# Performance work log

Measured on AMD Instinct MI355X. Metric: run time of the kernel, lower is better.

Reference implementation:

```python
import jax, jax.numpy as jnp
import numpy as np

IN_SIZE = 1024
OUT_SIZE = 4096
LOGN = 12          # ceil(log2(max(in,out)))
N = 1 << LOGN      # 4096
BATCH = 8192


def setup_inputs() -> dict:
    key = jax.random.key(0)
    k1, k2, k3 = jax.random.split(key, 3)
    # kaiming_uniform on [2*logN, N]: fan_in = N, bound = sqrt(6/fan_in)
    bound = float(np.sqrt(6.0 / N))
    learned_params = jax.random.uniform(k1, (2 * LOGN, N), minval=-bound, maxval=bound, dtype=jnp.float32)
    inp = jax.random.normal(k2, (BATCH, IN_SIZE), dtype=jnp.float32)
    # np.random.permutation(N)[:out_size]
    out_row_indices = jax.random.permutation(k3, N)[:OUT_SIZE].astype(jnp.int32)
    return {"input": inp, "learned_params": learned_params, "out_row_indices": out_row_indices}


def reference(input, learned_params, out_row_indices):
    # Build B = prod_i (diag(p[2i]) + P_i @ diag(p[2i+1])), P_i[j, j^2^i] = 1.
    # (P_i @ diag(d) @ B)[j, :] = d[j^2^i] * B[j^2^i, :], so each layer is a
    # row-scale + xor-permuted row-scale of B (same math as the dense matmul chain).
    B = jnp.eye(N, dtype=input.dtype)
    for i in range(LOGN):
        perm = jnp.arange(N) ^ (1 << i)  # static per layer
        B = learned_params[2 * i][:, None] * B + learned_params[2 * i + 1][perm][:, None] * B[perm]
    layer_matrix = B[out_row_indices, :IN_SIZE]   # [out_size, in_size]
    return input @ layer_matrix.T                  # [batch, out_size]
```

## Files before the change

kernel.cpp:

```cpp
#include <hip/hip_runtime.h>


typedef float f4 __attribute__((ext_vector_type(4)));
typedef float f2 __attribute__((ext_vector_type(2)));
typedef int   i4 __attribute__((ext_vector_type(4)));

__device__ __forceinline__ int swz(int e) {
    return e ^ (((e >> 5) & 3) << 2);
}

template<int CTRL>
__device__ __forceinline__ float dppx(float x) {
    int xi = __builtin_bit_cast(int, x);
    int r  = __builtin_amdgcn_update_dpp(xi, xi, CTRL, 0xF, 0xF, true);
    return __builtin_bit_cast(float, r);
}

__global__ void __launch_bounds__(256) bfly_prep(
    const float* __restrict__ lp, const int* __restrict__ orow,
    float* __restrict__ scale, int* __restrict__ src2)
{
    int j = blockIdx.x * 256 + threadIdx.x;
    if (j >= 4096) return;
    int r = orow[j];
    int c = r & 1023;
    int u = r & 2047;
    const float* A10 = lp + 20 * 4096;
    const float* B10 = lp + 21 * 4096;
    const float* A11 = lp + 22 * 4096;
    const float* B11 = lp + 23 * 4096;
    float f11 = (r & 2048) ? B11[u] : A11[u];
    float f10 = (r & 1024) ? B10[c] : A10[c];
    scale[j] = f11 * f10;
    src2[j] = c ^ (((c >> 4) & 7) << 1);
}

__global__ void __launch_bounds__(256, 4) bfly_main(
    const float* __restrict__ inp, const float* __restrict__ lp,
    const float* __restrict__ scale, const int* __restrict__ src2,
    float* __restrict__ out)
{
    __shared__ __align__(16) float cf[10 * 1024];
    const int t = threadIdx.x;
    const int wave = t >> 6, lane = t & 63;

    #pragma unroll
    for (int q = 0; q < 10; ++q) {
        const f4 v = *reinterpret_cast<const f4*>(lp + (size_t)(10 + q) * 4096 + t * 4);
        *reinterpret_cast<f4*>(&cf[q * 1024 + swz(t * 4)]) = v;
    }

    const int sBase = blockIdx.x * 8 + wave * 2;
    float x[2][16];
    #pragma unroll
    for (int m = 0; m < 2; ++m) {
        const f4* p = reinterpret_cast<const f4*>(inp + (size_t)(sBase + m) * 1024 + lane * 16);
        #pragma unroll
        for (int c = 0; c < 4; ++c) {
            f4 v = p[c];
            x[m][4*c+0] = v.x; x[m][4*c+1] = v.y; x[m][4*c+2] = v.z; x[m][4*c+3] = v.w;
        }
    }

    __syncthreads();

    #pragma unroll
    for (int i = 0; i < 4; ++i) {
        float a[16], b[16];
        const f4* A = reinterpret_cast<const f4*>(lp + (size_t)(2*i)   * 4096 + lane * 16);
        const f4* B = reinterpret_cast<const f4*>(lp + (size_t)(2*i+1) * 4096 + lane * 16);
        #pragma unroll
        for (int c = 0; c < 4; ++c) {
            f4 va = A[c], vb = B[c];
            a[4*c+0]=va.x; a[4*c+1]=va.y; a[4*c+2]=va.z; a[4*c+3]=va.w;
            b[4*c+0]=vb.x; b[4*c+1]=vb.y; b[4*c+2]=vb.z; b[4*c+3]=vb.w;
        }
        const int s = 1 << i;
        #pragma unroll
        for (int m = 0; m < 2; ++m) {
            #pragma unroll
            for (int k = 0; k < 16; ++k) {
                if (!(k & s)) {
                    float lo = x[m][k], hi = x[m][k | s];
                    x[m][k]     = a[k]     * lo + b[k | s] * hi;
                    x[m][k | s] = a[k | s] * hi + b[k]     * lo;
                }
            }
        }
    }

    {
        float a[16], b[16];
        const f4* A = reinterpret_cast<const f4*>(lp + (size_t)8 * 4096 + lane * 16);
        const f4* B = reinterpret_cast<const f4*>(lp + (size_t)9 * 4096 + (lane ^ 1) * 16);
        #pragma unroll
        for (int c = 0; c < 4; ++c) {
            f4 va = A[c], vb = B[c];
            a[4*c+0]=va.x; a[4*c+1]=va.y; a[4*c+2]=va.z; a[4*c+3]=va.w;
            b[4*c+0]=vb.x; b[4*c+1]=vb.y; b[4*c+2]=vb.z; b[4*c+3]=vb.w;
        }
        #pragma unroll
        for (int m = 0; m < 2; ++m)
            #pragma unroll
            for (int k = 0; k < 16; ++k) {
                float v = x[m][k];
                x[m][k] = a[k] * v + b[k] * dppx<0xB1>(v);
            }
    }

    #pragma unroll
    for (int i = 5; i < 10; ++i) {
        const int d = 1 << (i - 4);
        float a[16], b[16];
        const float* arow = &cf[(size_t)(i - 5) * 2048];
        const float* brow = arow + 1024;
        #pragma unroll
        for (int c = 0; c < 4; ++c) {
            f4 va = *reinterpret_cast<const f4*>(&arow[swz(lane * 16 + 4 * c)]);
            f4 vb = *reinterpret_cast<const f4*>(&brow[swz((lane ^ d) * 16 + 4 * c)]);
            a[4*c+0]=va.x; a[4*c+1]=va.y; a[4*c+2]=va.z; a[4*c+3]=va.w;
            b[4*c+0]=vb.x; b[4*c+1]=vb.y; b[4*c+2]=vb.z; b[4*c+3]=vb.w;
        }
        #pragma unroll
        for (int m = 0; m < 2; ++m) {
            #pragma unroll
            for (int k = 0; k < 16; ++k) {
                float v = x[m][k];
                float xp = (d == 2) ? dppx<0x4E>(v)
                         : (d == 8) ? dppx<0x128>(v)
                         :            __shfl_xor(v, d, 64);
                x[m][k] = a[k] * v + b[k] * xp;
            }
        }
    }

    __syncthreads();

    float* zz = &cf[(size_t)wave * 2048];
    const int km0 = (lane & 7) << 1;

    #pragma unroll
    for (int k = 0; k < 16; k += 2) {
        int pi = lane * 16 + (k ^ km0);
        f4 v = { x[0][k], x[1][k], x[0][k+1], x[1][k+1] };
        *reinterpret_cast<f4*>(&zz[2 * pi]) = v;
    }

    const i4* srv = reinterpret_cast<const i4*>(src2);
    const f4* scv = reinterpret_cast<const f4*>(scale);
    f4* o0 = reinterpret_cast<f4*>(out + (size_t)sBase * 4096);
    f4* o1 = reinterpret_cast<f4*>(out + (size_t)(sBase + 1) * 4096);

    i4 si = srv[lane];
    f4 sc = scv[lane];
    #pragma unroll
    for (int it = 0; it < 16; ++it) {
        i4 si_c = si;
        f4 sc_c = sc;
        if (it + 1 < 16) {
            si = srv[(it + 1) * 64 + lane];
            sc = scv[(it + 1) * 64 + lane];
        }
        int j4 = it * 64 + lane;
        f2 vx = *reinterpret_cast<const f2*>(&zz[2 * si_c.x]);
        f2 vy = *reinterpret_cast<const f2*>(&zz[2 * si_c.y]);
        f2 vz = *reinterpret_cast<const f2*>(&zz[2 * si_c.z]);
        f2 vw = *reinterpret_cast<const f2*>(&zz[2 * si_c.w]);
        f4 r0 = { sc_c.x * vx.x, sc_c.y * vy.x, sc_c.z * vz.x, sc_c.w * vw.x };
        f4 r1 = { sc_c.x * vx.y, sc_c.y * vy.y, sc_c.z * vz.y, sc_c.w * vw.y };
        o0[j4] = r0;
        o1[j4] = r1;
    }
}

extern "C" void kernel_launch(void* const* d_in, const int* in_sizes, int n_in,
                              void* d_out, int out_size, void* d_ws, size_t ws_size,
                              hipStream_t stream) {
    const float* inp  = (const float*)d_in[0];
    const float* lp   = (const float*)d_in[1];
    const int*   orow = (const int*)d_in[2];
    float* out = (float*)d_out;

    float* scale = (float*)d_ws;
    int*   src2  = (int*)((char*)d_ws + 4096 * 4);

    bfly_prep<<<16, 256, 0, stream>>>(lp, orow, scale, src2);
    bfly_main<<<1024, 256, 0, stream>>>(inp, lp, scale, src2, out);
}
```

Before: 44.60 us.

## Process four batch rows per wave with float4 LDS gather

```diff
diff --git a/kernel.cpp b/kernel.cpp
--- a/kernel.cpp
+++ b/kernel.cpp
@@ -2,7 +2,6 @@
 
 
 typedef float f4 __attribute__((ext_vector_type(4)));
-typedef float f2 __attribute__((ext_vector_type(2)));
 typedef int   i4 __attribute__((ext_vector_type(4)));
 
 __device__ __forceinline__ int swz(int e) {
@@ -18,7 +17,7 @@
 
 __global__ void __launch_bounds__(256) bfly_prep(
     const float* __restrict__ lp, const int* __restrict__ orow,
-    float* __restrict__ scale, int* __restrict__ src2)
+    float* __restrict__ scale, int* __restrict__ src4)
 {
     int j = blockIdx.x * 256 + threadIdx.x;
     if (j >= 4096) return;
@@ -32,28 +31,28 @@
     float f11 = (r & 2048) ? B11[u] : A11[u];
     float f10 = (r & 1024) ? B10[c] : A10[c];
     scale[j] = f11 * f10;
-    src2[j] = c ^ (((c >> 4) & 7) << 1);
+    src4[j] = c ^ ((c >> 4) & 7);
 }
 
-__global__ void __launch_bounds__(256, 4) bfly_main(
+__global__ void __launch_bounds__(256, 2) bfly_main(
     const float* __restrict__ inp, const float* __restrict__ lp,
-    const float* __restrict__ scale, const int* __restrict__ src2,
+    const float* __restrict__ scale, const int* __restrict__ src4,
     float* __restrict__ out)
 {
-    __shared__ __align__(16) float cf[10 * 1024];
+    __shared__ __align__(16) float smem[16384];
     const int t = threadIdx.x;
     const int wave = t >> 6, lane = t & 63;
 
     #pragma unroll
     for (int q = 0; q < 10; ++q) {
         const f4 v = *reinterpret_cast<const f4*>(lp + (size_t)(10 + q) * 4096 + t * 4);
-        *reinterpret_cast<f4*>(&cf[q * 1024 + swz(t * 4)]) = v;
+        *reinterpret_cast<f4*>(&smem[q * 1024 + swz(t * 4)]) = v;
     }
 
-    const int sBase = blockIdx.x * 8 + wave * 2;
-    float x[2][16];
+    const int sBase = blockIdx.x * 16 + wave * 4;
+    float x[4][16];
     #pragma unroll
-    for (int m = 0; m < 2; ++m) {
+    for (int m = 0; m < 4; ++m) {
         const f4* p = reinterpret_cast<const f4*>(inp + (size_t)(sBase + m) * 1024 + lane * 16);
         #pragma unroll
         for (int c = 0; c < 4; ++c) {
@@ -77,7 +76,7 @@
         }
         const int s = 1 << i;
         #pragma unroll
-        for (int m = 0; m < 2; ++m) {
+        for (int m = 0; m < 4; ++m) {
             #pragma unroll
             for (int k = 0; k < 16; ++k) {
                 if (!(k & s)) {
@@ -100,7 +99,7 @@
             b[4*c+0]=vb.x; b[4*c+1]=vb.y; b[4*c+2]=vb.z; b[4*c+3]=vb.w;
         }
         #pragma unroll
-        for (int m = 0; m < 2; ++m)
+        for (int m = 0; m < 4; ++m)
             #pragma unroll
             for (int k = 0; k < 16; ++k) {
                 float v = x[m][k];
@@ -112,7 +111,7 @@
     for (int i = 5; i < 10; ++i) {
         const int d = 1 << (i - 4);
         float a[16], b[16];
-        const float* arow = &cf[(size_t)(i - 5) * 2048];
+        const float* arow = &smem[(size_t)(i - 5) * 2048];
         const float* brow = arow + 1024;
         #pragma unroll
         for (int c = 0; c < 4; ++c) {
@@ -122,7 +121,7 @@
             b[4*c+0]=vb.x; b[4*c+1]=vb.y; b[4*c+2]=vb.z; b[4*c+3]=vb.w;
         }
         #pragma unroll
-        for (int m = 0; m < 2; ++m) {
+        for (int m = 0; m < 4; ++m) {
             #pragma unroll
             for (int k = 0; k < 16; ++k) {
                 float v = x[m][k];
@@ -136,20 +135,21 @@
 
     __syncthreads();
 
-    float* zz = &cf[(size_t)wave * 2048];
-    const int km0 = (lane & 7) << 1;
+    f4* zz = reinterpret_cast<f4*>(smem) + (size_t)wave * 1024;
 
+    const int km = lane & 7;
     #pragma unroll
-    for (int k = 0; k < 16; k += 2) {
-        int pi = lane * 16 + (k ^ km0);
-        f4 v = { x[0][k], x[1][k], x[0][k+1], x[1][k+1] };
-        *reinterpret_cast<f4*>(&zz[2 * pi]) = v;
+    for (int k = 0; k < 16; ++k) {
+        f4 v = { x[0][k], x[1][k], x[2][k], x[3][k] };
+        zz[(lane * 16 + k) ^ km] = v;
     }
 
-    const i4* srv = reinterpret_cast<const i4*>(src2);
+    const i4* srv = reinterpret_cast<const i4*>(src4);
     const f4* scv = reinterpret_cast<const f4*>(scale);
-    f4* o0 = reinterpret_cast<f4*>(out + (size_t)sBase * 4096);
+    f4* o0 = reinterpret_cast<f4*>(out + (size_t)(sBase + 0) * 4096);
     f4* o1 = reinterpret_cast<f4*>(out + (size_t)(sBase + 1) * 4096);
+    f4* o2 = reinterpret_cast<f4*>(out + (size_t)(sBase + 2) * 4096);
+    f4* o3 = reinterpret_cast<f4*>(out + (size_t)(sBase + 3) * 4096);
 
     i4 si = srv[lane];
     f4 sc = scv[lane];
@@ -162,14 +162,18 @@
             sc = scv[(it + 1) * 64 + lane];
         }
         int j4 = it * 64 + lane;
-        f2 vx = *reinterpret_cast<const f2*>(&zz[2 * si_c.x]);
-        f2 vy = *reinterpret_cast<const f2*>(&zz[2 * si_c.y]);
-        f2 vz = *reinterpret_cast<const f2*>(&zz[2 * si_c.z]);
-        f2 vw = *reinterpret_cast<const f2*>(&zz[2 * si_c.w]);
-        f4 r0 = { sc_c.x * vx.x, sc_c.y * vy.x, sc_c.z * vz.x, sc_c.w * vw.x };
-        f4 r1 = { sc_c.x * vx.y, sc_c.y * vy.y, sc_c.z * vz.y, sc_c.w * vw.y };
+        f4 vx = zz[si_c.x];
+        f4 vy = zz[si_c.y];
+        f4 vz = zz[si_c.z];
+        f4 vw = zz[si_c.w];
+        f4 r0 = { sc_c.x * vx[0], sc_c.y * vy[0], sc_c.z * vz[0], sc_c.w * vw[0] };
+        f4 r1 = { sc_c.x * vx[1], sc_c.y * vy[1], sc_c.z * vz[1], sc_c.w * vw[1] };
+        f4 r2 = { sc_c.x * vx[2], sc_c.y * vy[2], sc_c.z * vz[2], sc_c.w * vw[2] };
+        f4 r3 = { sc_c.x * vx[3], sc_c.y * vy[3], sc_c.z * vz[3], sc_c.w * vw[3] };
         o0[j4] = r0;
         o1[j4] = r1;
+        o2[j4] = r2;
+        o3[j4] = r3;
     }
 }
 
@@ -182,8 +186,8 @@
     float* out = (float*)d_out;
 
     float* scale = (float*)d_ws;
-    int*   src2  = (int*)((char*)d_ws + 4096 * 4);
+    int*   src4  = (int*)((char*)d_ws + 4096 * 4);
 
-    bfly_prep<<<16, 256, 0, stream>>>(lp, orow, scale, src2);
-    bfly_main<<<1024, 256, 0, stream>>>(inp, lp, scale, src2, out);
+    bfly_prep<<<16, 256, 0, stream>>>(lp, orow, scale, src4);
+    bfly_main<<<512, 256, 0, stream>>>(inp, lp, scale, src4, out);
 }
```

Result: slower. 46.55 us (+4.4%).

## Remap per-lane element layout to drop shared-memory coefficient staging and barriers

Applied to the files above, without the earlier changes.

```diff
diff --git a/kernel.cpp b/kernel.cpp
--- a/kernel.cpp
+++ b/kernel.cpp
@@ -4,10 +4,6 @@
 typedef float f4 __attribute__((ext_vector_type(4)));
 typedef float f2 __attribute__((ext_vector_type(2)));
 typedef int   i4 __attribute__((ext_vector_type(4)));
-
-__device__ __forceinline__ int swz(int e) {
-    return e ^ (((e >> 5) & 3) << 2);
-}
 
 template<int CTRL>
 __device__ __forceinline__ float dppx(float x) {
@@ -40,110 +36,112 @@
     const float* __restrict__ scale, const int* __restrict__ src2,
     float* __restrict__ out)
 {
-    __shared__ __align__(16) float cf[10 * 1024];
+    __shared__ __align__(16) float zb[4 * 2048];
     const int t = threadIdx.x;
     const int wave = t >> 6, lane = t & 63;
+    const int sBase = blockIdx.x * 8 + wave * 2;
 
-    #pragma unroll
-    for (int q = 0; q < 10; ++q) {
-        const f4 v = *reinterpret_cast<const f4*>(lp + (size_t)(10 + q) * 4096 + t * 4);
-        *reinterpret_cast<f4*>(&cf[q * 1024 + swz(t * 4)]) = v;
-    }
-
-    const int sBase = blockIdx.x * 8 + wave * 2;
     float x[2][16];
     #pragma unroll
     for (int m = 0; m < 2; ++m) {
-        const f4* p = reinterpret_cast<const f4*>(inp + (size_t)(sBase + m) * 1024 + lane * 16);
+        const float* row = inp + (size_t)(sBase + m) * 1024 + lane * 4;
         #pragma unroll
         for (int c = 0; c < 4; ++c) {
-            f4 v = p[c];
+            f4 v = *reinterpret_cast<const f4*>(row + c * 256);
             x[m][4*c+0] = v.x; x[m][4*c+1] = v.y; x[m][4*c+2] = v.z; x[m][4*c+3] = v.w;
         }
     }
 
-    __syncthreads();
-
     #pragma unroll
-    for (int i = 0; i < 4; ++i) {
+    for (int i = 0; i < 2; ++i) {
         float a[16], b[16];
-        const f4* A = reinterpret_cast<const f4*>(lp + (size_t)(2*i)   * 4096 + lane * 16);
-        const f4* B = reinterpret_cast<const f4*>(lp + (size_t)(2*i+1) * 4096 + lane * 16);
+        const float* A = lp + (size_t)(2*i)   * 4096 + lane * 4;
+        const float* B = lp + (size_t)(2*i+1) * 4096 + lane * 4;
         #pragma unroll
         for (int c = 0; c < 4; ++c) {
-            f4 va = A[c], vb = B[c];
+            f4 va = *reinterpret_cast<const f4*>(A + c * 256);
+            f4 vb = *reinterpret_cast<const f4*>(B + c * 256);
             a[4*c+0]=va.x; a[4*c+1]=va.y; a[4*c+2]=va.z; a[4*c+3]=va.w;
             b[4*c+0]=vb.x; b[4*c+1]=vb.y; b[4*c+2]=vb.z; b[4*c+3]=vb.w;
         }
-        const int s = 1 << i;
+        const int sr = 1 << i;
         #pragma unroll
         for (int m = 0; m < 2; ++m) {
             #pragma unroll
-            for (int k = 0; k < 16; ++k) {
-                if (!(k & s)) {
-                    float lo = x[m][k], hi = x[m][k | s];
-                    x[m][k]     = a[k]     * lo + b[k | s] * hi;
-                    x[m][k | s] = a[k | s] * hi + b[k]     * lo;
+            for (int r = 0; r < 16; ++r) {
+                if (!(r & sr)) {
+                    float lo = x[m][r], hi = x[m][r | sr];
+                    x[m][r]      = a[r]      * lo + b[r | sr] * hi;
+                    x[m][r | sr] = a[r | sr] * hi + b[r]      * lo;
                 }
             }
         }
     }
 
-    {
+    #pragma unroll
+    for (int i = 2; i < 8; ++i) {
+        const int d = 1 << (i - 2);
         float a[16], b[16];
-        const f4* A = reinterpret_cast<const f4*>(lp + (size_t)8 * 4096 + lane * 16);
-        const f4* B = reinterpret_cast<const f4*>(lp + (size_t)9 * 4096 + (lane ^ 1) * 16);
+        const float* A = lp + (size_t)(2*i)   * 4096 + lane * 4;
+        const float* B = lp + (size_t)(2*i+1) * 4096 + (lane ^ d) * 4;
         #pragma unroll
         for (int c = 0; c < 4; ++c) {
-            f4 va = A[c], vb = B[c];
-            a[4*c+0]=va.x; a[4*c+1]=va.y; a[4*c+2]=va.z; a[4*c+3]=va.w;
-            b[4*c+0]=vb.x; b[4*c+1]=vb.y; b[4*c+2]=vb.z; b[4*c+3]=vb.w;
-        }
-        #pragma unroll
-        for (int m = 0; m < 2; ++m)
-            #pragma unroll
-            for (int k = 0; k < 16; ++k) {
-                float v = x[m][k];
-                x[m][k] = a[k] * v + b[k] * dppx<0xB1>(v);
-            }
-    }
-
-    #pragma unroll
-    for (int i = 5; i < 10; ++i) {
-        const int d = 1 << (i - 4);
-        float a[16], b[16];
-        const float* arow = &cf[(size_t)(i - 5) * 2048];
-        const float* brow = arow + 1024;
-        #pragma unroll
-        for (int c = 0; c < 4; ++c) {
-            f4 va = *reinterpret_cast<const f4*>(&arow[swz(lane * 16 + 4 * c)]);
-            f4 vb = *reinterpret_cast<const f4*>(&brow[swz((lane ^ d) * 16 + 4 * c)]);
+            f4 va = *reinterpret_cast<const f4*>(A + c * 256);
+            f4 vb = *reinterpret_cast<const f4*>(B + c * 256);
             a[4*c+0]=va.x; a[4*c+1]=va.y; a[4*c+2]=va.z; a[4*c+3]=va.w;
             b[4*c+0]=vb.x; b[4*c+1]=vb.y; b[4*c+2]=vb.z; b[4*c+3]=vb.w;
         }
         #pragma unroll
         for (int m = 0; m < 2; ++m) {
             #pragma unroll
-            for (int k = 0; k < 16; ++k) {
-                float v = x[m][k];
-                float xp = (d == 2) ? dppx<0x4E>(v)
+            for (int r = 0; r < 16; ++r) {
+                float v = x[m][r];
+                float xp = (d == 1) ? dppx<0xB1>(v)
+                         : (d == 2) ? dppx<0x4E>(v)
                          : (d == 8) ? dppx<0x128>(v)
                          :            __shfl_xor(v, d, 64);
-                x[m][k] = a[k] * v + b[k] * xp;
+                x[m][r] = a[r] * v + b[r] * xp;
             }
         }
     }
 
-    __syncthreads();
+    #pragma unroll
+    for (int i = 8; i < 10; ++i) {
+        float a[16], b[16];
+        const float* A = lp + (size_t)(2*i)   * 4096 + lane * 4;
+        const float* B = lp + (size_t)(2*i+1) * 4096 + lane * 4;
+        #pragma unroll
+        for (int c = 0; c < 4; ++c) {
+            f4 va = *reinterpret_cast<const f4*>(A + c * 256);
+            f4 vb = *reinterpret_cast<const f4*>(B + c * 256);
+            a[4*c+0]=va.x; a[4*c+1]=va.y; a[4*c+2]=va.z; a[4*c+3]=va.w;
+            b[4*c+0]=vb.x; b[4*c+1]=vb.y; b[4*c+2]=vb.z; b[4*c+3]=vb.w;
+        }
+        const int sr = 1 << (i - 6);
+        #pragma unroll
+        for (int m = 0; m < 2; ++m) {
+            #pragma unroll
+            for (int r = 0; r < 16; ++r) {
+                if (!(r & sr)) {
+                    float lo = x[m][r], hi = x[m][r | sr];
+                    x[m][r]      = a[r]      * lo + b[r | sr] * hi;
+                    x[m][r | sr] = a[r | sr] * hi + b[r]      * lo;
+                }
+            }
+        }
+    }
 
-    float* zz = &cf[(size_t)wave * 2048];
-    const int km0 = (lane & 7) << 1;
-
+    float* zw = &zb[wave * 2048];
+    const int sw = (lane & 28) >> 1;
     #pragma unroll
-    for (int k = 0; k < 16; k += 2) {
-        int pi = lane * 16 + (k ^ km0);
-        f4 v = { x[0][k], x[1][k], x[0][k+1], x[1][k+1] };
-        *reinterpret_cast<f4*>(&zz[2 * pi]) = v;
+    for (int c = 0; c < 4; ++c) {
+        #pragma unroll
+        for (int e = 0; e < 4; e += 2) {
+            int r = 4 * c + e;
+            int slot = (c * 256 + lane * 4 + e) ^ sw;
+            f4 v = { x[0][r], x[1][r], x[0][r+1], x[1][r+1] };
+            *reinterpret_cast<f4*>(&zw[2 * slot]) = v;
+        }
     }
 
     const i4* srv = reinterpret_cast<const i4*>(src2);
@@ -162,10 +160,10 @@
             sc = scv[(it + 1) * 64 + lane];
         }
         int j4 = it * 64 + lane;
-        f2 vx = *reinterpret_cast<const f2*>(&zz[2 * si_c.x]);
-        f2 vy = *reinterpret_cast<const f2*>(&zz[2 * si_c.y]);
-        f2 vz = *reinterpret_cast<const f2*>(&zz[2 * si_c.z]);
-        f2 vw = *reinterpret_cast<const f2*>(&zz[2 * si_c.w]);
+        f2 vx = *reinterpret_cast<const f2*>(&zw[2 * si_c.x]);
+        f2 vy = *reinterpret_cast<const f2*>(&zw[2 * si_c.y]);
+        f2 vz = *reinterpret_cast<const f2*>(&zw[2 * si_c.z]);
+        f2 vw = *reinterpret_cast<const f2*>(&zw[2 * si_c.w]);
         f4 r0 = { sc_c.x * vx.x, sc_c.y * vy.x, sc_c.z * vz.x, sc_c.w * vw.x };
         f4 r1 = { sc_c.x * vx.y, sc_c.y * vy.y, sc_c.z * vz.y, sc_c.w * vw.y };
         o0[j4] = r0;
```

Result: slower. 76.63 us (+71.8%).
